# Performance work log

Hardware: AMD Instinct MI355X
Metric: run time of the kernel (lower is better)

## Reference

```python
import jax, jax.numpy as jnp
import numpy as np

GROUPS = 8
OUT_C = 64
IN_C = 64
N, T, V = 64, 128, 25
NS = 3
JOINTS = jnp.array([3, 20, 7, 11, 14, 18])  # part-skeleton joints selected in forward


def setup_inputs() -> dict:
    key = jax.random.key(0)
    ks = jax.random.split(key, 24)

    def kaiming(k, shape, fan):
        return jax.random.normal(k, shape, dtype=jnp.float32) * np.float32((2.0 / fan) ** 0.5)

    A = jax.random.uniform(ks[0], (NS, V, V), dtype=jnp.float32)
    PA = jax.random.uniform(ks[1], (NS, 6, 6), dtype=jnp.float32)
    pa = jnp.tile(PA[:, None], (1, GROUPS, 1, 1))       # buffer [3,G,6,6]
    A1buf = jnp.tile(A[:, None], (1, GROUPS, 1, 1))     # buffer [3,G,25,25]
    inp = {
        "x": jax.random.normal(ks[2], (N, IN_C, T, V), dtype=jnp.float32),
        "Decouplepap": pa,          # param initialized identically to buffer
        "pa": pa,
        "DecoupleA": A1buf,
        "A1buf": A1buf,
        "Wp": kaiming(ks[3], (OUT_C // 8, IN_C), OUT_C // 8), "bp": jnp.zeros((OUT_C // 8,), jnp.float32),
        "Ws": kaiming(ks[4], (OUT_C, IN_C), OUT_C), "bs": jnp.zeros((OUT_C,), jnp.float32),
        "W1": kaiming(ks[5], (OUT_C // 8 * 3, OUT_C // 8), OUT_C // 8 * 3), "b1": jnp.zeros((OUT_C // 8 * 3,), jnp.float32),
        "W2": kaiming(ks[6], (OUT_C * 3, OUT_C), OUT_C * 3), "b2": jnp.zeros((OUT_C * 3,), jnp.float32),
        "We": kaiming(ks[7], (OUT_C, OUT_C // 8), OUT_C), "be": jnp.zeros((OUT_C,), jnp.float32),
        # Conv1d(1,1,k=1,bias=False) weights are scalars
        "w_t1": jax.random.normal(ks[8], (), jnp.float32),
        "w_t2": jax.random.normal(ks[9], (), jnp.float32),
        "w_tw1": jax.random.normal(ks[10], (), jnp.float32),
        "w_tw2": jax.random.normal(ks[11], (), jnp.float32),
        "w_tw11": jax.random.normal(ks[12], (), jnp.float32),
        "w_tw21": jax.random.normal(ks[13], (), jnp.float32),
        "w_s1": jax.random.normal(ks[14], (), jnp.float32),
        "w_s2": jax.random.normal(ks[15], (), jnp.float32),
        "k_ca": jax.random.normal(ks[16], (3,), jnp.float32) * 0.5,  # conv2_1 kernel (k=3, pad=1)
        "bn_g": jnp.full((OUT_C,), 1e-6, jnp.float32),  # bn_init(bn, 1e-6)
        "bn_b": jnp.zeros((OUT_C,), jnp.float32),
    }
    return inp


def reference(x, Decouplepap, pa, DecoupleA, A1buf, Wp, bp, Ws, bs, W1, b1, W2, b2,
              We, be, w_t1, w_t2, w_tw1, w_tw2, w_tw11, w_tw21, w_s1, w_s2,
              k_ca, bn_g, bn_b):
    relu = jax.nn.relu
    n, c, t, v = x.shape
    out_c = Ws.shape[0]
    groups = pa.shape[1]
    ns = pa.shape[0]

    def conv1x1(h, W, b):  # Conv2d 1x1: [n,c,t,v] x [o,c] -> [n,o,t,v]
        return jnp.einsum('nctv,oc->notv', h, W) + b[None, :, None, None]

    # learned adjacencies: buffer + param, tiled over channel groups
    nlp = jnp.tile(Decouplepap + pa, (1, out_c // groups // 8, 1, 1))   # [3, out//8, 6, 6]
    nlA = jnp.tile(A1buf + DecoupleA, (1, out_c // groups, 1, 1))       # [3, out, 25, 25]

    x1 = conv1x1(x, Wp, bp)   # [n, out//8, t, 25]
    x2 = conv1x1(x, Ws, bs)   # [n, out, t, 25]
    x1_part = x1[:, :, :, JOINTS]  # [n, out//8, t, 6]

    # part<->joint attention (avg-pool over c,t then scalar conv1d + relu)
    a1 = relu(w_t1 * x1_part.mean((1, 2)))  # [n,6]
    a2 = relu(w_t2 * x1.mean((1, 2)))       # [n,25]
    A12 = jax.nn.softmax(a1[:, :, None] * a2[:, None, :], axis=-2)  # [n,6,25], softmax over dim 6
    x1_GCN = jnp.einsum('nctv,nqv->nctq', x1, A12)  # [n, out//8, t, 6]

    # subset loop collapses: atten identical across subsets
    xm = x1_GCN.mean((1, 2))  # [n,6]
    att = jax.nn.softmax(relu(w_tw1 * xm)[:, :, None] * relu(w_tw2 * xm)[:, None, :], axis=-2)
    x1_final = 0.5 * att[:, None, None] + nlp[None]  # [n,3,out//8,6,6]

    m = conv1x1(x1_GCN, W1, b1).reshape(n, ns, out_c // 8, t, 6)
    y = jnp.einsum('nkctv,nkcvw->nctw', m, x1_final)  # [n, out//8, t, 6]

    xm2 = x2.mean((1, 2))  # [n,25]
    att2 = jax.nn.softmax(relu(w_tw11 * xm2)[:, :, None] * relu(w_tw21 * xm2)[:, None, :], axis=-2)
    A_final = 0.5 * att2[:, None, None] + nlA[None]  # [n,3,out,25,25]

    m2 = conv1x1(x2, W2, b2).reshape(n, ns, out_c, t, v)
    y1 = jnp.einsum('nkctv,nkcvw->nctw', m2, A_final)  # [n, out, t, 25]

    # fuse part branch into joint branch
    a1l = relu(w_s1 * y.mean((1, 2)))   # [n,6]
    a2l = relu(w_s2 * y1.mean((1, 2)))  # [n,25]
    A12l = jax.nn.softmax(a1l[:, :, None] * a2l[:, None, :], axis=-2)  # [n,6,25]
    yl = conv1x1(jnp.einsum('nctv,nvq->nctq', y, A12l), We, be)  # [n, out, t, 25]
    y = 0.5 * yl + y1

    # ECA-style channel gate: conv1d(k=3,pad=1) over pooled channels
    q = y.mean((2, 3))  # [n, out]
    qp = jnp.pad(q, ((0, 0), (1, 1)))
    qc = k_ca[0] * qp[:, :-2] + k_ca[1] * qp[:, 1:-1] + k_ca[2] * qp[:, 2:]
    y = y * jax.nn.sigmoid(qc)[:, :, None, None] + y

    # BatchNorm2d (training-mode batch stats, biased var, eps=1e-5)
    mu = y.mean((0, 2, 3), keepdims=True)
    var = ((y - mu) ** 2).mean((0, 2, 3), keepdims=True)
    y = (y - mu) / jnp.sqrt(var + 1e-5) * bn_g[None, :, None, None] + bn_b[None, :, None, None]

    # residual (in_channels == out_channels -> identity down)
    return relu(y + x)
```

## Files before the change

kernel.cpp:

```cpp
#include <hip/hip_runtime.h>
#include <math.h>

#define NN 64
#define CC 64
#define TT 128
#define VV 25
#define NSK 3
#define G8 8

#define OFF_XMEAN  0
#define OFF_A12    102400
#define OFF_ATT2   112000
#define OFF_ATT    152000
#define OFF_X1GCN  154304
#define OFF_Y      547520
#define OFF_A12L   940736
#define OFF_W2EFF  950336
#define OFF_B2EFF  962624
#define OFF_XMSUM  962816
#define OFF_YSUM   963200
#define OFF_Y1SUM  963584
#define OFF_QSUM   965184
#define OFF_Q2SUM  969280
#define OFF_ALPHA  973376
#define OFF_BETA   977472
#define ACC_START  OFF_XMSUM
#define ACC_LEN    (OFF_ALPHA - OFF_XMSUM)

__global__ __launch_bounds__(64) void k_xmean(const float* __restrict__ x, float* __restrict__ xmean){
  int nc = blockIdx.x;
  const float* p = x + (size_t)nc*TT*VV;
  float acc[VV];
  #pragma unroll
  for (int v=0;v<VV;++v) acc[v]=0.f;
  for (int t = threadIdx.x; t < TT; t += 64){
    const float* row = p + t*VV;
    #pragma unroll
    for (int v=0; v<VV; ++v) acc[v] += row[v];
  }
  #pragma unroll
  for (int v=0; v<VV; ++v){
    float a = acc[v];
    #pragma unroll
    for (int off=32; off; off>>=1) a += __shfl_down(a, off, 64);
    acc[v]=a;
  }
  if (threadIdx.x==0){
    #pragma unroll
    for (int v=0;v<VV;++v) xmean[nc*VV+v] = acc[v]*(1.f/TT);
  }
}

__global__ __launch_bounds__(64) void k_w2eff(const float* __restrict__ W2, const float* __restrict__ Ws,
    const float* __restrict__ bs, const float* __restrict__ b2,
    float* __restrict__ W2eff, float* __restrict__ b2eff){
  int o = blockIdx.x, cc = threadIdx.x;
  float s = 0.f, sb = 0.f;
  for (int c1=0;c1<CC;++c1){ float w = W2[o*CC+c1]; s += w*Ws[c1*CC+cc]; sb += w*bs[c1]; }
  W2eff[o*CC+cc] = s;
  if (cc==0) b2eff[o] = sb + b2[o];
}

__global__ __launch_bounds__(64) void k_attn1(const float* __restrict__ xmean,
    const float* __restrict__ Wp, const float* __restrict__ bp,
    const float* __restrict__ Ws, const float* __restrict__ bs,
    const float* __restrict__ w_t1, const float* __restrict__ w_t2,
    const float* __restrict__ w_tw11, const float* __restrict__ w_tw21,
    float* __restrict__ A12, float* __restrict__ att2){
  int n = blockIdx.x, tid = threadIdx.x;
  __shared__ float wpbar[CC], wsbar[CC];
  __shared__ float a2pre[VV], a2[VV], r1[VV], r2[VV], a1[6];
  {
    float s=0.f, s2=0.f;
    for (int o=0;o<G8;++o) s += Wp[o*CC+tid];
    for (int o=0;o<CC;++o) s2 += Ws[o*CC+tid];
    wpbar[tid]=s*(1.f/G8); wsbar[tid]=s2*(1.f/CC);
  }
  __syncthreads();
  float bpbar=0.f, bsbar=0.f;
  for (int o=0;o<G8;++o) bpbar += bp[o];
  bpbar *= (1.f/G8);
  for (int o=0;o<CC;++o) bsbar += bs[o];
  bsbar *= (1.f/CC);
  if (tid < VV){
    float s1=0.f, s2=0.f;
    const float* xm = xmean + n*CC*VV + tid;
    for (int c=0;c<CC;++c){ float xv = xm[c*VV]; s1 += xv*wpbar[c]; s2 += xv*wsbar[c]; }
    float ap = s1 + bpbar, xm2v = s2 + bsbar;
    a2pre[tid] = ap;
    a2[tid] = fmaxf(0.f, w_t2[0]*ap);
    r1[tid] = fmaxf(0.f, w_tw11[0]*xm2v);
    r2[tid] = fmaxf(0.f, w_tw21[0]*xm2v);
  }
  __syncthreads();
  if (tid < 6){
    const int J[6]={3,20,7,11,14,18};
    a1[tid] = fmaxf(0.f, w_t1[0]*a2pre[J[tid]]);
  }
  __syncthreads();
  if (tid < VV){
    float m=-1e30f;
    #pragma unroll
    for (int q=0;q<6;++q) m = fmaxf(m, a1[q]*a2[tid]);
    float e[6]; float s=0.f;
    #pragma unroll
    for (int q=0;q<6;++q){ e[q]=__expf(a1[q]*a2[tid]-m); s+=e[q]; }
    float inv=1.f/s;
    #pragma unroll
    for (int q=0;q<6;++q) A12[(n*6+q)*VV+tid] = e[q]*inv;
    float m2=-1e30f;
    for (int v=0;v<VV;++v) m2 = fmaxf(m2, r1[v]*r2[tid]);
    float s2=0.f;
    for (int v=0;v<VV;++v) s2 += __expf(r1[v]*r2[tid]-m2);
    float inv2=1.f/s2;
    for (int v=0;v<VV;++v) att2[(n*VV+v)*VV+tid] = __expf(r1[v]*r2[tid]-m2)*inv2;
  }
}

__global__ __launch_bounds__(256) void k_x1gcn(const float* __restrict__ x,
    const float* __restrict__ Wp, const float* __restrict__ bp,
    const float* __restrict__ A12, float* __restrict__ x1gcn, float* __restrict__ xmsum){
  __shared__ float xs[CC][200];
  __shared__ float x1s[G8][200];
  __shared__ float A12s[6][VV];
  __shared__ float Wps[G8][CC];
  __shared__ float qb[6];
  int n = blockIdx.x >> 4;
  int t0 = (blockIdx.x & 15) * 8;
  int tid = threadIdx.x;
  if (tid < 6*VV) A12s[tid/VV][tid%VV] = A12[n*6*VV + tid];
  if (tid >= 6*VV && tid < 6*VV+6) qb[tid - 6*VV] = 0.f;
  for (int f=tid; f<G8*CC; f+=256) Wps[f>>6][f&63] = Wp[f];
  const float* xb = x + (size_t)n*CC*TT*VV + t0*VV;
  for (int f=tid; f<CC*200; f+=256){
    int c = f/200, j = f - c*200;
    xs[c][j] = xb[c*TT*VV + j];
  }
  __syncthreads();
  for (int f=tid; f<G8*200; f+=256){
    int o = f/200, j = f - o*200;
    float s = bp[o];
    #pragma unroll 16
    for (int c=0;c<CC;++c) s += xs[c][j]*Wps[o][c];
    x1s[o][j] = s;
  }
  __syncthreads();
  float* xg = x1gcn + ((size_t)n*G8*TT + t0)*6;
  for (int f=tid; f<G8*48; f+=256){
    int o=f/48, r=f-o*48, tl=r/6, q=r-tl*6;
    const float* xr = &x1s[o][tl*VV];
    float s=0.f;
    #pragma unroll
    for (int v=0;v<VV;++v) s += xr[v]*A12s[q][v];
    xg[o*TT*6 + tl*6 + q] = s;
    atomicAdd(&qb[q], s);
  }
  __syncthreads();
  if (tid<6) atomicAdd(&xmsum[n*6+tid], qb[tid]);
}

__global__ __launch_bounds__(64) void k_att(const float* __restrict__ xmsum,
    const float* __restrict__ w_tw1, const float* __restrict__ w_tw2, float* __restrict__ att){
  int n=blockIdx.x, tid=threadIdx.x;
  __shared__ float aa[6], bb[6];
  if (tid<6){
    float xm = xmsum[n*6+tid]*(1.f/(G8*TT));
    aa[tid]=fmaxf(0.f, w_tw1[0]*xm);
    bb[tid]=fmaxf(0.f, w_tw2[0]*xm);
  }
  __syncthreads();
  if (tid<6){
    float m=-1e30f;
    #pragma unroll
    for(int i=0;i<6;++i) m=fmaxf(m, aa[i]*bb[tid]);
    float e[6]; float s=0.f;
    #pragma unroll
    for(int i=0;i<6;++i){ e[i]=__expf(aa[i]*bb[tid]-m); s+=e[i]; }
    float inv=1.f/s;
    #pragma unroll
    for(int i=0;i<6;++i) att[(n*6+i)*6+tid]=e[i]*inv;
  }
}

__global__ __launch_bounds__(256) void k_y(const float* __restrict__ x1gcn,
    const float* __restrict__ W1, const float* __restrict__ b1,
    const float* __restrict__ att, const float* __restrict__ Dpap, const float* __restrict__ pa,
    float* __restrict__ y, float* __restrict__ ysum){
  __shared__ float xg[G8][192];
  __shared__ float ms[24][192];
  __shared__ float F[NSK][G8][36];
  __shared__ float W1s[24][G8];
  __shared__ float ysb[6];
  int n = blockIdx.x >> 2;
  int t0 = (blockIdx.x & 3) * 32;
  int tid = threadIdx.x;
  float* Ff = &F[0][0][0];
  for (int f=tid; f<NSK*G8*36; f+=256){
    int ij = f % 36;
    Ff[f] = 0.5f*att[n*36+ij] + Dpap[f] + pa[f];
  }
  if (tid < 24*G8) W1s[tid/G8][tid%G8] = W1[tid];
  if (tid < 6) ysb[tid] = 0.f;
  const float* xgb = x1gcn + ((size_t)n*G8*TT + t0)*6;
  for (int f=tid; f<G8*192; f+=256){
    int o=f/192, j=f-o*192;
    xg[o][j] = xgb[o*TT*6 + j];
  }
  __syncthreads();
  for (int f=tid; f<24*192; f+=256){
    int o=f/192, j=f-o*192;
    float s = b1[o];
    #pragma unroll
    for (int c=0;c<G8;++c) s += xg[c][j]*W1s[o][c];
    ms[o][j] = s;
  }
  __syncthreads();
  float* yb = y + ((size_t)n*G8*TT + t0)*6;
  for (int f=tid; f<G8*192; f+=256){
    int c=f/192, r=f-c*192, tl=r/6, w=r-tl*6;
    float s=0.f;
    #pragma unroll
    for (int k=0;k<NSK;++k){
      #pragma unroll
      for (int v=0;v<6;++v) s += ms[k*G8+c][tl*6+v]*F[k][c][v*6+w];
    }
    yb[c*TT*6 + r] = s;
    atomicAdd(&ysb[w], s);
  }
  __syncthreads();
  if (tid<6) atomicAdd(&ysum[n*6+tid], ysb[tid]);
}

__global__ __launch_bounds__(256) void k_y1(const float* __restrict__ x,
    const float* __restrict__ W2eff, const float* __restrict__ b2eff,
    const float* __restrict__ att2, const float* __restrict__ A1buf, const float* __restrict__ DecA,
    float* __restrict__ y1, float* __restrict__ y1sum){
  __shared__ __align__(16) float xT[100][68];
  __shared__ float E[G8][VV*VV];
  __shared__ float y1sb[VV];
  int n = blockIdx.x >> 5;
  int t0 = (blockIdx.x & 31) * 4;
  int tid = threadIdx.x;
  int c = tid & 63;
  int tl = tid >> 6;
  const float* xb = x + (size_t)n*CC*TT*VV + t0*VV;
  for (int f = tid; f < CC*100; f += 256){
    int cc = f/100, tv = f - cc*100;
    xT[tv][cc] = xb[cc*TT*VV + tv];
  }
  if (tid < VV) y1sb[tid] = 0.f;
  float acc[VV];
  #pragma unroll
  for (int w=0;w<VV;++w) acc[w]=0.f;
  float* Ef = &E[0][0];
  for (int k=0;k<NSK;++k){
    __syncthreads();
    for (int f=tid; f<G8*VV*VV; f+=256){
      Ef[f] = 0.5f*att2[n*VV*VV + (f % (VV*VV))] + A1buf[k*G8*VV*VV + f] + DecA[k*G8*VV*VV + f];
    }
    float w2r[CC];
    const float4* wr = (const float4*)&W2eff[(k*CC + c)*CC];
    #pragma unroll
    for (int j=0;j<16;++j){
      float4 t4 = wr[j];
      w2r[4*j+0]=t4.x; w2r[4*j+1]=t4.y; w2r[4*j+2]=t4.z; w2r[4*j+3]=t4.w;
    }
    float bk = b2eff[k*CC + c];
    __syncthreads();
    const float* Eg = &E[c & 7][0];
    for (int v=0; v<VV; ++v){
      const float4* xr = (const float4*)&xT[tl*VV + v][0];
      float m2 = bk;
      #pragma unroll
      for (int j=0;j<16;++j){
        float4 xv = xr[j];
        m2 += xv.x*w2r[4*j+0] + xv.y*w2r[4*j+1] + xv.z*w2r[4*j+2] + xv.w*w2r[4*j+3];
      }
      const float* Ev = Eg + v*VV;
      #pragma unroll
      for (int w=0;w<VV;++w) acc[w] += m2 * Ev[w];
    }
  }
  float* yb = y1 + (size_t)n*CC*TT*VV + t0*VV;
  #pragma unroll
  for (int w=0;w<VV;++w) yb[c*TT*VV + tl*VV + w] = acc[w];
  #pragma unroll
  for (int w=0;w<VV;++w){
    float a = acc[w];
    #pragma unroll
    for (int off=32; off; off>>=1) a += __shfl_down(a, off, 64);
    if ((tid & 63)==0) atomicAdd(&y1sb[w], a);
  }
  __syncthreads();
  if (tid < VV) atomicAdd(&y1sum[n*VV+tid], y1sb[tid]);
}

__global__ __launch_bounds__(64) void k_a12l(const float* __restrict__ ysum, const float* __restrict__ y1sum,
    const float* __restrict__ w_s1, const float* __restrict__ w_s2, float* __restrict__ A12l){
  int n=blockIdx.x, tid=threadIdx.x;
  __shared__ float a1l[6], a2l[VV];
  if (tid<6) a1l[tid] = fmaxf(0.f, w_s1[0]*ysum[n*6+tid]*(1.f/(G8*TT)));
  if (tid<VV) a2l[tid] = fmaxf(0.f, w_s2[0]*y1sum[n*VV+tid]*(1.f/(CC*TT)));
  __syncthreads();
  if (tid<VV){
    float m=-1e30f;
    #pragma unroll
    for(int q=0;q<6;++q) m=fmaxf(m, a1l[q]*a2l[tid]);
    float e[6]; float s=0.f;
    #pragma unroll
    for(int q=0;q<6;++q){ e[q]=__expf(a1l[q]*a2l[tid]-m); s+=e[q]; }
    float inv=1.f/s;
    #pragma unroll
    for(int q=0;q<6;++q) A12l[(n*6+q)*VV+tid] = e[q]*inv;
  }
}

__global__ __launch_bounds__(256) void k_yprime(const float* __restrict__ y,
    const float* __restrict__ A12l, const float* __restrict__ We, const float* __restrict__ be,
    float* __restrict__ yp, float* __restrict__ qsum, float* __restrict__ q2sum){
  __shared__ float ys[G8][24];
  __shared__ float Al[6][VV];
  __shared__ float WesT[G8][CC];
  __shared__ float z[G8][4][VV];
  __shared__ float qb[CC], q2b[CC];
  int n = blockIdx.x >> 5;
  int t0 = (blockIdx.x & 31) * 4;
  int tid = threadIdx.x;
  int c = tid & 63, tl = tid >> 6;
  if (tid < 6*VV) Al[tid/VV][tid%VV] = A12l[n*6*VV + tid];
  for (int f=tid; f<CC*G8; f+=256) WesT[f&7][f>>3] = We[f];
  if (tid < G8*24){ int o=tid/24, j=tid-o*24; ys[o][j] = y[((size_t)(n*G8+o)*TT + t0)*6 + j]; }
  if (tid < CC){ qb[tid]=0.f; q2b[tid]=0.f; }
  __syncthreads();
  for (int f=tid; f<G8*4*VV; f+=256){
    int o=f/100, r=f-o*100, t=r/VV, w=r-t*VV;
    float s=0.f;
    #pragma unroll
    for (int v=0;v<6;++v) s += ys[o][t*6+v]*Al[v][w];
    z[o][t][w]=s;
  }
  __syncthreads();
  float* yb = yp + ((size_t)n*CC + c)*TT*VV + (t0+tl)*VV;
  float qs=0.f, q2s=0.f;
  float bec = be[c];
  #pragma unroll
  for (int w=0;w<VV;++w){
    float s = bec;
    #pragma unroll
    for (int o=0;o<G8;++o) s += z[o][tl][w]*WesT[o][c];
    float val = 0.5f*s + yb[w];
    yb[w] = val;
    qs += val; q2s += val*val;
  }
  atomicAdd(&qb[c], qs); atomicAdd(&q2b[c], q2s);
  __syncthreads();
  if (tid < CC){ atomicAdd(&qsum[n*CC+tid], qb[tid]); atomicAdd(&q2sum[n*CC+tid], q2b[tid]); }
}

__global__ __launch_bounds__(256) void k_bnparams(const float* __restrict__ qsum, const float* __restrict__ q2sum,
    const float* __restrict__ k_ca, const float* __restrict__ bn_g, const float* __restrict__ bn_b,
    float* __restrict__ alpha, float* __restrict__ beta){
  __shared__ float gg[NN*CC];
  __shared__ float qm[NN*CC];
  __shared__ float scale_s[CC];
  int tid = threadIdx.x;
  for (int f=tid; f<NN*CC; f+=256) qm[f] = qsum[f]*(1.f/(TT*VV));
  __syncthreads();
  float k0=k_ca[0], k1=k_ca[1], k2=k_ca[2];
  for (int f=tid; f<NN*CC; f+=256){
    int cch = f & 63;
    float qm1 = cch>0  ? qm[f-1] : 0.f;
    float qp1 = cch<63 ? qm[f+1] : 0.f;
    float qc = k0*qm1 + k1*qm[f] + k2*qp1;
    gg[f] = 1.f + 1.f/(1.f+__expf(-qc));
  }
  __syncthreads();
  if (tid < CC){
    float mu=0.f, e2=0.f;
    for (int nn=0; nn<NN; ++nn){
      float g = gg[nn*CC+tid];
      mu += g * qm[nn*CC+tid];
      e2 += g*g*q2sum[nn*CC+tid];
    }
    mu *= (1.f/NN);
    e2 *= (1.f/(NN*TT*VV));
    float var = e2 - mu*mu;
    float sc = bn_g[tid]*rsqrtf(var+1e-5f);
    scale_s[tid]=sc;
    beta[tid] = bn_b[tid] - mu*sc;
  }
  __syncthreads();
  for (int f=tid; f<NN*CC; f+=256) alpha[f] = gg[f]*scale_s[f & 63];
}

__global__ __launch_bounds__(256) void k_final(const float* __restrict__ x,
    const float* __restrict__ alpha, const float* __restrict__ beta,
    float* __restrict__ out){
  int i = blockIdx.x*256 + threadIdx.x;
  const float4* x4 = (const float4*)x;
  float4* o4 = (float4*)out;
  float4 xv = x4[i];
  float4 yv = o4[i];
  int nc = i / 800;
  float a = alpha[nc], b = beta[nc & 63];
  float4 r;
  r.x = fmaxf(0.f, yv.x*a + b + xv.x);
  r.y = fmaxf(0.f, yv.y*a + b + xv.y);
  r.z = fmaxf(0.f, yv.z*a + b + xv.z);
  r.w = fmaxf(0.f, yv.w*a + b + xv.w);
  o4[i] = r;
}

extern "C" void kernel_launch(void* const* d_in, const int* in_sizes, int n_in,
                              void* d_out, int out_size, void* d_ws, size_t ws_size,
                              hipStream_t stream) {
  const float* x    = (const float*)d_in[0];
  const float* Dpap = (const float*)d_in[1];
  const float* pa   = (const float*)d_in[2];
  const float* DecA = (const float*)d_in[3];
  const float* A1buf= (const float*)d_in[4];
  const float* Wp   = (const float*)d_in[5];
  const float* bp   = (const float*)d_in[6];
  const float* Ws   = (const float*)d_in[7];
  const float* bs   = (const float*)d_in[8];
  const float* W1   = (const float*)d_in[9];
  const float* b1   = (const float*)d_in[10];
  const float* W2   = (const float*)d_in[11];
  const float* b2   = (const float*)d_in[12];
  const float* We   = (const float*)d_in[13];
  const float* be   = (const float*)d_in[14];
  const float* w_t1 = (const float*)d_in[15];
  const float* w_t2 = (const float*)d_in[16];
  const float* w_tw1  = (const float*)d_in[17];
  const float* w_tw2  = (const float*)d_in[18];
  const float* w_tw11 = (const float*)d_in[19];
  const float* w_tw21 = (const float*)d_in[20];
  const float* w_s1 = (const float*)d_in[21];
  const float* w_s2 = (const float*)d_in[22];
  const float* k_ca = (const float*)d_in[23];
  const float* bn_g = (const float*)d_in[24];
  const float* bn_b = (const float*)d_in[25];
  float* out = (float*)d_out;
  float* ws  = (float*)d_ws;

  float* xmean = ws + OFF_XMEAN;
  float* A12   = ws + OFF_A12;
  float* att2  = ws + OFF_ATT2;
  float* att   = ws + OFF_ATT;
  float* x1gcn = ws + OFF_X1GCN;
  float* yv    = ws + OFF_Y;
  float* A12l  = ws + OFF_A12L;
  float* w2eff = ws + OFF_W2EFF;
  float* b2eff = ws + OFF_B2EFF;
  float* xmsum = ws + OFF_XMSUM;
  float* ysum  = ws + OFF_YSUM;
  float* y1sum = ws + OFF_Y1SUM;
  float* qsum  = ws + OFF_QSUM;
  float* q2sum = ws + OFF_Q2SUM;
  float* alpha = ws + OFF_ALPHA;
  float* beta  = ws + OFF_BETA;

  hipMemsetAsync(ws + ACC_START, 0, ACC_LEN*sizeof(float), stream);

  k_w2eff<<<192, 64, 0, stream>>>(W2, Ws, bs, b2, w2eff, b2eff);
  k_xmean<<<NN*CC, 64, 0, stream>>>(x, xmean);
  k_attn1<<<NN, 64, 0, stream>>>(xmean, Wp, bp, Ws, bs, w_t1, w_t2, w_tw11, w_tw21, A12, att2);
  k_y1<<<NN*32, 256, 0, stream>>>(x, w2eff, b2eff, att2, A1buf, DecA, out, y1sum);
  k_x1gcn<<<NN*16, 256, 0, stream>>>(x, Wp, bp, A12, x1gcn, xmsum);
  k_att<<<NN, 64, 0, stream>>>(xmsum, w_tw1, w_tw2, att);
  k_y<<<NN*4, 256, 0, stream>>>(x1gcn, W1, b1, att, Dpap, pa, yv, ysum);
  k_a12l<<<NN, 64, 0, stream>>>(ysum, y1sum, w_s1, w_s2, A12l);
  k_yprime<<<NN*32, 256, 0, stream>>>(yv, A12l, We, be, out, qsum, q2sum);
  k_bnparams<<<1, 256, 0, stream>>>(qsum, q2sum, k_ca, bn_g, bn_b, alpha, beta);
  k_final<<<(NN*CC*TT*VV)/1024, 256, 0, stream>>>(x, alpha, beta, out);
}
```

Baseline: 539.4 us.

## Transpose x to channel-last and precompute fused adjacency for y1 branch

Adds a kernel that transposes x into a [n,t,v,c] layout so the y1 kernel can read contiguous float4 vectors, plus a kernel that precomputes the combined adjacency 0.5*att2 + A1buf + DecA per (n,k,g) padded to 28 columns. A new y1 kernel then computes the 1x1 conv with register-held weights and applies the graph aggregation per thread over two time steps. It also outputs y1 and its sums via atomics. The extra transpose pass adds about 52MB of global traffic and depends on the workspace being large enough; otherwise the old path runs.

```diff
diff --git a/kernel.cpp b/kernel.cpp
--- a/kernel.cpp
+++ b/kernel.cpp
@@ -26,6 +26,9 @@
 #define OFF_BETA   977472
 #define ACC_START  OFF_XMSUM
 #define ACC_LEN    (OFF_ALPHA - OFF_XMSUM)
+#define OFF_EG     977536
+#define OFF_XT     2052736
+#define WS_NEED_FLOATS (OFF_XT + 13107200)
 
 __global__ __launch_bounds__(64) void k_xmean(const float* __restrict__ x, float* __restrict__ xmean){
   int nc = blockIdx.x;
@@ -114,6 +117,106 @@
     for (int v=0;v<VV;++v) s2 += __expf(r1[v]*r2[tid]-m2);
     float inv2=1.f/s2;
     for (int v=0;v<VV;++v) att2[(n*VV+v)*VV+tid] = __expf(r1[v]*r2[tid]-m2)*inv2;
+  }
+}
+
+__global__ __launch_bounds__(256) void k_xT(const float* __restrict__ x, float* __restrict__ xT){
+  __shared__ float xs[CC][201];
+  int n = blockIdx.x >> 4;
+  int t0 = (blockIdx.x & 15) * 8;
+  int tid = threadIdx.x;
+  const float* xb = x + (size_t)n*CC*TT*VV + t0*VV;
+  for (int f=tid; f<CC*200; f+=256){
+    int c = f/200, j = f - c*200;
+    xs[c][j] = xb[c*TT*VV + j];
+  }
+  __syncthreads();
+  float* ob = xT + (size_t)(n*TT + t0)*VV*64;
+  for (int f=tid; f<200*64; f+=256){
+    int tv = f >> 6, c = f & 63;
+    ob[f] = xs[c][tv];
+  }
+}
+
+__global__ __launch_bounds__(256) void k_eprep(const float* __restrict__ att2,
+    const float* __restrict__ A1buf, const float* __restrict__ DecA, float* __restrict__ Eg){
+  int f = blockIdx.x*256 + threadIdx.x;
+  int w = f % 28;
+  int r = f / 28;
+  int v = r % 25;
+  int r2 = r / 25;
+  int g = r2 & 7;
+  int r3 = r2 >> 3;
+  int k = r3 % 3;
+  int n = r3 / 3;
+  float val = 0.f;
+  if (w < 25){
+    int si = ((k*G8+g)*VV+v)*VV + w;
+    val = 0.5f*att2[n*VV*VV + v*VV + w] + A1buf[si] + DecA[si];
+  }
+  Eg[f] = val;
+}
+
+__global__ __launch_bounds__(256,2) void k_y1b(const float* __restrict__ xT,
+    const float* __restrict__ W2eff, const float* __restrict__ b2eff,
+    const float* __restrict__ Eg, float* __restrict__ y1, float* __restrict__ y1sum){
+  int n = blockIdx.x >> 4;
+  int t0 = (blockIdx.x & 15) * 8;
+  int tid = threadIdx.x;
+  int c = tid & 63;
+  int wv = tid >> 6;
+  int tA = __builtin_amdgcn_readfirstlane(t0 + 2*wv);
+  float acc[2][VV];
+  #pragma unroll
+  for (int w=0;w<VV;++w){ acc[0][w]=0.f; acc[1][w]=0.f; }
+  const float4* xrA0 = (const float4*)(xT + (size_t)(n*TT + tA)*VV*64);
+  const float4* xrB0 = (const float4*)(xT + (size_t)(n*TT + tA + 1)*VV*64);
+  #pragma unroll 1
+  for (int k=0;k<NSK;++k){
+    float w2r[CC];
+    const float4* wr = (const float4*)&W2eff[(k*CC + c)*CC];
+    #pragma unroll
+    for (int j=0;j<16;++j){
+      float4 t4 = wr[j];
+      w2r[4*j+0]=t4.x; w2r[4*j+1]=t4.y; w2r[4*j+2]=t4.z; w2r[4*j+3]=t4.w;
+    }
+    float bk = b2eff[k*CC + c];
+    const float4* Ev0 = (const float4*)(Eg + ((size_t)(n*NSK + k)*G8 + (c&7))*700);
+    #pragma unroll 1
+    for (int v=0; v<VV; ++v){
+      const float4* xa = xrA0 + v*16;
+      const float4* xb = xrB0 + v*16;
+      float ma = bk, mb = bk;
+      #pragma unroll
+      for (int j=0;j<16;++j){
+        float4 a4 = xa[j];
+        float4 b4 = xb[j];
+        ma += a4.x*w2r[4*j+0] + a4.y*w2r[4*j+1] + a4.z*w2r[4*j+2] + a4.w*w2r[4*j+3];
+        mb += b4.x*w2r[4*j+0] + b4.y*w2r[4*j+1] + b4.z*w2r[4*j+2] + b4.w*w2r[4*j+3];
+      }
+      const float4* Ev = Ev0 + v*7;
+      #pragma unroll
+      for (int w4=0; w4<6; ++w4){
+        float4 e = Ev[w4];
+        acc[0][4*w4+0] += ma*e.x; acc[1][4*w4+0] += mb*e.x;
+        acc[0][4*w4+1] += ma*e.y; acc[1][4*w4+1] += mb*e.y;
+        acc[0][4*w4+2] += ma*e.z; acc[1][4*w4+2] += mb*e.z;
+        acc[0][4*w4+3] += ma*e.w; acc[1][4*w4+3] += mb*e.w;
+      }
+      { float4 e = Ev[6]; acc[0][24] += ma*e.x; acc[1][24] += mb*e.x; }
+    }
+  }
+  float* yb = y1 + ((size_t)n*CC + c)*TT*VV;
+  #pragma unroll
+  for (int w=0;w<VV;++w){ yb[tA*VV + w] = acc[0][w]; }
+  #pragma unroll
+  for (int w=0;w<VV;++w){ yb[(tA+1)*VV + w] = acc[1][w]; }
+  #pragma unroll
+  for (int w=0;w<VV;++w){
+    float a = acc[0][w] + acc[1][w];
+    #pragma unroll
+    for (int off=32; off; off>>=1) a += __shfl_down(a, off, 64);
+    if (c==0) atomicAdd(&y1sum[n*VV+w], a);
   }
 }
 
@@ -459,13 +562,23 @@
   float* q2sum = ws + OFF_Q2SUM;
   float* alpha = ws + OFF_ALPHA;
   float* beta  = ws + OFF_BETA;
+  float* Eg    = ws + OFF_EG;
+  float* xT    = ws + OFF_XT;
+
+  bool bigws = ws_size >= (size_t)WS_NEED_FLOATS * sizeof(float);
 
   hipMemsetAsync(ws + ACC_START, 0, ACC_LEN*sizeof(float), stream);
 
   k_w2eff<<<192, 64, 0, stream>>>(W2, Ws, bs, b2, w2eff, b2eff);
   k_xmean<<<NN*CC, 64, 0, stream>>>(x, xmean);
   k_attn1<<<NN, 64, 0, stream>>>(xmean, Wp, bp, Ws, bs, w_t1, w_t2, w_tw11, w_tw21, A12, att2);
-  k_y1<<<NN*32, 256, 0, stream>>>(x, w2eff, b2eff, att2, A1buf, DecA, out, y1sum);
+  if (bigws){
+    k_xT<<<NN*16, 256, 0, stream>>>(x, xT);
+    k_eprep<<<4200, 256, 0, stream>>>(att2, A1buf, DecA, Eg);
+    k_y1b<<<NN*16, 256, 0, stream>>>(xT, w2eff, b2eff, Eg, out, y1sum);
+  } else {
+    k_y1<<<NN*32, 256, 0, stream>>>(x, w2eff, b2eff, att2, A1buf, DecA, out, y1sum);
+  }
   k_x1gcn<<<NN*16, 256, 0, stream>>>(x, Wp, bp, A12, x1gcn, xmsum);
   k_att<<<NN, 64, 0, stream>>>(xmsum, w_tw1, w_tw2, att);
   k_y<<<NN*4, 256, 0, stream>>>(x1gcn, W1, b1, att, Dpap, pa, yv, ysum);
```

Result: slower. 587.4 us (+8.9%).
